# Kernel optimization log

Hardware: AMD Instinct MI355X
Metric: run time of the kernel (lower is better)

## Reference

```python
import jax, jax.numpy as jnp
import numpy as np

HIDDEN = 1024
HEADS = 16
HEAD_DIM = HIDDEN // HEADS


def setup_inputs() -> dict:
    key = jax.random.key(0)
    ks = jax.random.split(key, 12)
    B, S, D = 4, 2048, HIDDEN
    scale = 1.0 / np.sqrt(D)
    inp = {
        'q': jax.random.normal(ks[0], (B, S, D), jnp.float32),
        'k': jax.random.normal(ks[1], (B, S, D), jnp.float32),
        'v': jax.random.normal(ks[2], (B, S, D), jnp.float32),
        'Wq': jax.random.normal(ks[3], (D, D), jnp.float32) * scale,
        'bq': jnp.zeros((D,), jnp.float32),
        'Wk': jax.random.normal(ks[4], (D, D), jnp.float32) * scale,
        'bk': jnp.zeros((D,), jnp.float32),
        'Wv': jax.random.normal(ks[5], (D, D), jnp.float32) * scale,
        'bv': jnp.zeros((D,), jnp.float32),
        'Wo': jax.random.normal(ks[6], (D, D), jnp.float32) * scale,
        'bo': jnp.zeros((D,), jnp.float32),
    }
    return inp


def reference(q, k, v, Wq, bq, Wk, bk, Wv, bv, Wo, bo):
    B, S, D = q.shape
    H, Dh = HEADS, HEAD_DIM
    # QKV projections (weights stored as [in, out])
    Q = q @ Wq + bq
    K = k @ Wk + bk
    V = v @ Wv + bv
    # [B, H, S, Dh]
    Qh = Q.reshape(B, S, H, Dh).transpose(0, 2, 1, 3)
    Kh = K.reshape(B, S, H, Dh).transpose(0, 2, 1, 3)
    Vh = V.reshape(B, S, H, Dh).transpose(0, 2, 1, 3)
    # scaled dot-product attention, full [B,H,S,S] scores as in source
    scores = jnp.einsum('bhqd,bhkd->bhqk', Qh, Kh) / jnp.sqrt(jnp.float32(Dh))
    attn = jax.nn.softmax(scores, axis=-1)
    ctx = jnp.einsum('bhqk,bhkd->bhqd', attn, Vh)
    out = ctx.transpose(0, 2, 1, 3).reshape(B, S, D)
    return out @ Wo + bo
```

## Files before the change

### kernel.cpp

```cpp
#include <hip/hip_runtime.h>
#include <hip/hip_bf16.h>

#define HID 1024
#define NH 16
#define DH 64
#define NB 4
#define SQ 2048

typedef __bf16 bf16x8 __attribute__((ext_vector_type(8)));
typedef __bf16 bf16x2 __attribute__((ext_vector_type(2)));
typedef float f32x4 __attribute__((ext_vector_type(4)));
typedef float f32x16 __attribute__((ext_vector_type(16)));
typedef unsigned int u32x4 __attribute__((ext_vector_type(4)));

static __device__ __forceinline__ unsigned pkbf(float a, float b) {
  bf16x2 t; t[0] = (__bf16)a; t[1] = (__bf16)b;
  return __builtin_bit_cast(unsigned, t);
}

static __device__ __forceinline__ void gload16(const void* g, void* l) {
  __builtin_amdgcn_global_load_lds(
      (const __attribute__((address_space(1))) unsigned int*)g,
      (__attribute__((address_space(3))) unsigned int*)l, 16, 0, 0);
}

static __device__ __forceinline__ int xcd_swz(int lin, int nwg) {
  return (lin & 7) * (nwg >> 3) + (lin >> 3);
}

__global__ __launch_bounds__(256) void transpose_wf4_kernel(
    const float* __restrict__ Wq, const float* __restrict__ Wk,
    const float* __restrict__ Wv, const float* __restrict__ Wo,
    __bf16* __restrict__ Wcatf, __bf16* __restrict__ Wof) {
  const int which = blockIdx.z;
  const float* W = which == 0 ? Wq : (which == 1 ? Wk : (which == 2 ? Wv : Wo));
  __bf16* Wf = which == 3 ? Wof : Wcatf + (size_t)which * HID * HID;
  const int nblk = blockIdx.x, kt = blockIdx.y;
  const int tid = threadIdx.x, lane = tid & 63, wid = tid >> 6;
  const int fr = lane & 15, g = lane >> 4;
#pragma unroll
  for (int c = 0; c < 2; ++c) {
    const int wn_i = wid + c * 4;
    const int wn = wn_i >> 2, i = wn_i & 3;
    const int n = nblk * 128 + wn * 64 + i * 16 + fr;
    const int kb = kt * 32 + g * 8;
    bf16x8 v;
#pragma unroll
    for (int e = 0; e < 8; ++e)
      v[e] = (__bf16)W[(size_t)(kb + e) * HID + n];
    *reinterpret_cast<bf16x8*>(
        &Wf[(size_t)(nblk * 32 + kt) * 4096 + wn * 2048 + i * 512 + lane * 8]) = v;
  }
}

__global__ __launch_bounds__(256) void gemm_qkv_kernel(
    const float* __restrict__ Aq, const float* __restrict__ Ak,
    const float* __restrict__ Av, const __bf16* __restrict__ Wcatf,
    const float* __restrict__ bq, const float* __restrict__ bk,
    const float* __restrict__ bv, __bf16* __restrict__ Qh,
    __bf16* __restrict__ Kh, __bf16* __restrict__ Vt, float qscale) {
  const int K = HID;
  __shared__ __align__(16) char As2[2][10240];
  const int tid = threadIdx.x;
  const int lane = tid & 63;
  const int wid = tid >> 6;
  const int wm = wid >> 1, wn = wid & 1;
  const int lin = blockIdx.x + 24 * blockIdx.y;
  const int work = xcd_swz(lin, 1536);
  const int seg = work >> 9;
  const int rem = work & 511;
  const int m0 = (rem >> 3) * 128;
  const int nblk = seg * 8 + (rem & 7);
  const int n0 = nblk * 128;
  const int fr = lane & 15, g = lane >> 4;

  const float* Abase = seg == 0 ? Aq : (seg == 1 ? Ak : Av);
  const float* asrc =
      Abase + (size_t)(m0 + wid * 32 + (lane >> 3)) * K + (lane & 7) * 4;
  const __bf16* wsrc = Wcatf + (size_t)nblk * 32 * 4096 + wn * 2048 + lane * 8;

  const int awrow = wid * 32 + (lane >> 3);
  const int awcol = (lane & 7) * 8;

  float4 areg[4];
  auto loadA = [&](int kt) {
#pragma unroll
    for (int j = 0; j < 4; ++j)
      areg[j] = *reinterpret_cast<const float4*>(
          asrc + (size_t)j * 8 * K + kt * 32);
  };
  auto writeA = [&](int buf) {
#pragma unroll
    for (int j = 0; j < 4; ++j) {
      uint2 w;
      w.x = pkbf(areg[j].x, areg[j].y);
      w.y = pkbf(areg[j].z, areg[j].w);
      *reinterpret_cast<uint2*>(&As2[buf][(awrow + j * 8) * 80 + awcol]) = w;
    }
  };
  auto loadB = [&](int kt, bf16x8* br) {
    const __bf16* bp = wsrc + (size_t)kt * 4096;
#pragma unroll
    for (int i = 0; i < 4; ++i)
      br[i] = *reinterpret_cast<const bf16x8*>(bp + i * 512);
  };
  auto readA = [&](int buf, bf16x8* af) {
    const char* ac = &As2[buf][0];
#pragma unroll
    for (int i = 0; i < 4; ++i)
      af[i] = *reinterpret_cast<const bf16x8*>(
          ac + (wm * 64 + i * 16 + fr) * 80 + g * 16);
  };

  f32x4 acc[4][4] = {};
  const int NT = K / 32;
  bf16x8 bE[4], bO[4];
  loadA(0);
  writeA(0);
  loadB(0, bE);
  __syncthreads();
  int cur = 0;
  for (int kt = 0; kt < NT; kt += 2) {
    loadA(kt + 1);
    loadB(kt + 1, bO);
    {
      bf16x8 af[4];
      readA(cur, af);
#pragma unroll
      for (int i = 0; i < 4; ++i)
#pragma unroll
        for (int j = 0; j < 4; ++j)
          acc[i][j] = __builtin_amdgcn_mfma_f32_16x16x32_bf16(
              af[i], bE[j], acc[i][j], 0, 0, 0);
    }
    writeA(cur ^ 1);
    __syncthreads();
    cur ^= 1;
    if (kt + 2 < NT) {
      loadA(kt + 2);
      loadB(kt + 2, bE);
    }
    {
      bf16x8 af[4];
      readA(cur, af);
#pragma unroll
      for (int i = 0; i < 4; ++i)
#pragma unroll
        for (int j = 0; j < 4; ++j)
          acc[i][j] = __builtin_amdgcn_mfma_f32_16x16x32_bf16(
              af[i], bO[j], acc[i][j], 0, 0, 0);
    }
    if (kt + 2 < NT) {
      writeA(cur ^ 1);
      __syncthreads();
      cur ^= 1;
    }
  }

  const float* bias = seg == 0 ? bq : (seg == 1 ? bk : bv);
  const float oscale = seg == 0 ? qscale : 1.f;
#pragma unroll
  for (int i = 0; i < 4; ++i) {
#pragma unroll
    for (int j = 0; j < 4; ++j) {
      const int n = n0 + wn * 64 + j * 16 + fr;
      const int nn = n & 1023;
      const float bn = bias[nn];
      const int h = nn >> 6, dh = nn & (DH - 1);
#pragma unroll
      for (int r = 0; r < 4; ++r) {
        const int m = m0 + wm * 64 + i * 16 + g * 4 + r;
        const float v = (acc[i][j][r] + bn) * oscale;
        const int b = m >> 11, s = m & (SQ - 1);
        if (seg == 0) {
          Qh[(((size_t)(b * NH + h) * SQ) + s) * DH + dh] = (__bf16)v;
        } else if (seg == 1) {
          const int kvt = s >> 5, ql = s & 31;
          const int ds = dh >> 4, hi = (dh >> 3) & 1, e = dh & 7;
          Kh[(size_t)(b * NH + h) * SQ * DH +
             (size_t)kvt * 2048 + ds * 512 + (hi * 32 + ql) * 8 + e] = (__bf16)v;
        } else {
          const int i64 = s >> 6, c16 = (s >> 4) & 3;
          const int hi = (s >> 2) & 1, e = (s & 3) + 4 * ((s >> 3) & 1);
          const int dblk = dh >> 5, ql = dh & 31;
          Vt[(size_t)(b * NH + h) * SQ * DH +
             (size_t)i64 * 4096 + dblk * 2048 + c16 * 512 +
             (hi * 32 + ql) * 8 + e] = (__bf16)v;
        }
      }
    }
  }
}

__global__ __launch_bounds__(256) void gemm_out_kernel(
    const __bf16* __restrict__ Ap, const __bf16* __restrict__ Wof,
    const float* __restrict__ bias, float* __restrict__ out,
    int M, int N, int K) {
  __shared__ __align__(16) char Asm[2][8192];
  const int tid = threadIdx.x;
  const int lane = tid & 63;
  const int wid = tid >> 6;
  const int wm = wid >> 1, wn = wid & 1;
  const int gx = N / 128;
  const int lin = blockIdx.x + gx * blockIdx.y;
  const int work = xcd_swz(lin, gx * (M / 128));
  const int m0 = (work / gx) * 128, nblk = work % gx, n0 = nblk * 128;
  const int fr = lane & 15, g = lane >> 4, kg = (lane >> 4) * 8;

  const __bf16* abf = Ap + (size_t)(m0 + wid * 32 + (lane >> 2)) * K + (lane & 3) * 8;
  const __bf16* wsrc = Wof + (size_t)nblk * 32 * 4096 + wn * 2048 + lane * 8;

  auto stageA = [&](int buf, int kt) {
    char* ab = &Asm[buf][0] + wid * 2048;
#pragma unroll
    for (int j = 0; j < 2; ++j)
      gload16(abf + (size_t)j * 16 * K + kt * 32, ab + j * 1024);
  };
  auto loadB = [&](int kt, bf16x8* br) {
    const __bf16* bp = wsrc + (size_t)kt * 4096;
#pragma unroll
    for (int i = 0; i < 4; ++i)
      br[i] = *reinterpret_cast<const bf16x8*>(bp + i * 512);
  };
  auto readA = [&](int buf, bf16x8* af) {
    const char* ac = &Asm[buf][0];
#pragma unroll
    for (int i = 0; i < 4; ++i)
      af[i] = *reinterpret_cast<const bf16x8*>(
          ac + (wm * 64 + i * 16 + fr) * 64 + kg * 2);
  };

  f32x4 acc[4][4] = {};
  const int NT = K / 32;
  bf16x8 bE[4], bO[4];
  stageA(0, 0);
  loadB(0, bE);
  __syncthreads();
  int cur = 0;
  for (int kt = 0; kt < NT; kt += 2) {
    stageA(cur ^ 1, kt + 1);
    loadB(kt + 1, bO);
    {
      bf16x8 af[4];
      readA(cur, af);
#pragma unroll
      for (int i = 0; i < 4; ++i)
#pragma unroll
        for (int j = 0; j < 4; ++j)
          acc[i][j] = __builtin_amdgcn_mfma_f32_16x16x32_bf16(
              af[i], bE[j], acc[i][j], 0, 0, 0);
    }
    __syncthreads();
    cur ^= 1;
    if (kt + 2 < NT) {
      stageA(cur ^ 1, kt + 2);
      loadB(kt + 2, bE);
    }
    {
      bf16x8 af[4];
      readA(cur, af);
#pragma unroll
      for (int i = 0; i < 4; ++i)
#pragma unroll
        for (int j = 0; j < 4; ++j)
          acc[i][j] = __builtin_amdgcn_mfma_f32_16x16x32_bf16(
              af[i], bO[j], acc[i][j], 0, 0, 0);
    }
    if (kt + 2 < NT) {
      __syncthreads();
      cur ^= 1;
    }
  }

#pragma unroll
  for (int i = 0; i < 4; ++i) {
#pragma unroll
    for (int j = 0; j < 4; ++j) {
      const int n = n0 + wn * 64 + j * 16 + fr;
      const float bn = bias[n];
#pragma unroll
      for (int r = 0; r < 4; ++r) {
        const int m = m0 + wm * 64 + i * 16 + g * 4 + r;
        out[(size_t)m * N + n] = acc[i][j][r] + bn;
      }
    }
  }
}

__global__ __launch_bounds__(256) void attn_kernel(
    const __bf16* __restrict__ Q, const __bf16* __restrict__ K,
    const __bf16* __restrict__ V, __bf16* __restrict__ ctx) {
  __shared__ float tb[4][32][33];
  const int tid = threadIdx.x, lane = tid & 63, wid = tid >> 6;
  const int lin = blockIdx.x + 16 * blockIdx.y;
  const int work = xcd_swz(lin, 16 * NB * NH);
  const int bh = work >> 4;
  const int q0 = (work & 15) * 128 + wid * 32;
  const int ql = lane & 31, hi = lane >> 5;
  const __bf16* Qb = Q + (size_t)bh * SQ * DH;
  const __bf16* Kf = K + (size_t)bh * SQ * DH;
  const __bf16* Vf = V + (size_t)bh * SQ * DH;

  bf16x8 qf[4];
#pragma unroll
  for (int ds = 0; ds < 4; ++ds)
    qf[ds] = *reinterpret_cast<const bf16x8*>(
        &Qb[(size_t)(q0 + ql) * DH + ds * 16 + hi * 8]);

  f32x16 ot0 = {}, ot1 = {};
  float l_run = 0.f;

  for (int kv0 = 0; kv0 < SQ; kv0 += 64) {
    const __bf16* Ka = Kf + (size_t)(kv0 >> 5) * 2048 + lane * 8;
    const __bf16* Kc = Ka + 2048;
    bf16x8 kfa0 = *reinterpret_cast<const bf16x8*>(Ka);
    bf16x8 kfa1 = *reinterpret_cast<const bf16x8*>(Ka + 512);
    bf16x8 kfa2 = *reinterpret_cast<const bf16x8*>(Ka + 1024);
    bf16x8 kfa3 = *reinterpret_cast<const bf16x8*>(Ka + 1536);
    bf16x8 kfb0 = *reinterpret_cast<const bf16x8*>(Kc);
    bf16x8 kfb1 = *reinterpret_cast<const bf16x8*>(Kc + 512);
    bf16x8 kfb2 = *reinterpret_cast<const bf16x8*>(Kc + 1024);
    bf16x8 kfb3 = *reinterpret_cast<const bf16x8*>(Kc + 1536);
    const __bf16* Vbase = Vf + (size_t)(kv0 >> 6) * 4096 + lane * 8;
    bf16x8 v00a = *reinterpret_cast<const bf16x8*>(Vbase);
    bf16x8 v01a = *reinterpret_cast<const bf16x8*>(Vbase + 512);
    bf16x8 v00b = *reinterpret_cast<const bf16x8*>(Vbase + 1024);
    bf16x8 v01b = *reinterpret_cast<const bf16x8*>(Vbase + 1536);
    bf16x8 v10a = *reinterpret_cast<const bf16x8*>(Vbase + 2048);
    bf16x8 v11a = *reinterpret_cast<const bf16x8*>(Vbase + 2560);
    bf16x8 v10b = *reinterpret_cast<const bf16x8*>(Vbase + 3072);
    bf16x8 v11b = *reinterpret_cast<const bf16x8*>(Vbase + 3584);

    f32x16 sa = {}, sb = {};
    __builtin_amdgcn_s_setprio(1);
    sa = __builtin_amdgcn_mfma_f32_32x32x16_bf16(kfa0, qf[0], sa, 0, 0, 0);
    sb = __builtin_amdgcn_mfma_f32_32x32x16_bf16(kfb0, qf[0], sb, 0, 0, 0);
    sa = __builtin_amdgcn_mfma_f32_32x32x16_bf16(kfa1, qf[1], sa, 0, 0, 0);
    sb = __builtin_amdgcn_mfma_f32_32x32x16_bf16(kfb1, qf[1], sb, 0, 0, 0);
    sa = __builtin_amdgcn_mfma_f32_32x32x16_bf16(kfa2, qf[2], sa, 0, 0, 0);
    sb = __builtin_amdgcn_mfma_f32_32x32x16_bf16(kfb2, qf[2], sb, 0, 0, 0);
    sa = __builtin_amdgcn_mfma_f32_32x32x16_bf16(kfa3, qf[3], sa, 0, 0, 0);
    sb = __builtin_amdgcn_mfma_f32_32x32x16_bf16(kfb3, qf[3], sb, 0, 0, 0);
    __builtin_amdgcn_s_setprio(0);

    float pa[16], pb_[16];
#pragma unroll
    for (int r = 0; r < 16; ++r) pa[r] = __builtin_amdgcn_exp2f(sa[r]);
#pragma unroll
    for (int r = 0; r < 16; ++r) pb_[r] = __builtin_amdgcn_exp2f(sb[r]);
    {
      float u0 = 0.f, u1 = 0.f, u2 = 0.f, u3 = 0.f;
#pragma unroll
      for (int r = 0; r < 4; ++r) {
        u0 += pa[r] + pa[r + 4];
        u1 += pa[r + 8] + pa[r + 12];
        u2 += pb_[r] + pb_[r + 4];
        u3 += pb_[r + 8] + pb_[r + 12];
      }
      l_run += (u0 + u1) + (u2 + u3);
    }
    unsigned ca[8], cb[8];
#pragma unroll
    for (int i = 0; i < 8; ++i) {
      ca[i] = pkbf(pa[2 * i], pa[2 * i + 1]);
      cb[i] = pkbf(pb_[2 * i], pb_[2 * i + 1]);
    }
    u32x4 WA0, WA1, WB0, WB1;
    WA0[0] = ca[0]; WA0[1] = ca[1]; WA0[2] = ca[2]; WA0[3] = ca[3];
    WA1[0] = ca[4]; WA1[1] = ca[5]; WA1[2] = ca[6]; WA1[3] = ca[7];
    WB0[0] = cb[0]; WB0[1] = cb[1]; WB0[2] = cb[2]; WB0[3] = cb[3];
    WB1[0] = cb[4]; WB1[1] = cb[5]; WB1[2] = cb[6]; WB1[3] = cb[7];
    bf16x8 pa0 = __builtin_bit_cast(bf16x8, WA0);
    bf16x8 pa1 = __builtin_bit_cast(bf16x8, WA1);
    bf16x8 pb0 = __builtin_bit_cast(bf16x8, WB0);
    bf16x8 pb1 = __builtin_bit_cast(bf16x8, WB1);
    __builtin_amdgcn_s_setprio(1);
    ot0 = __builtin_amdgcn_mfma_f32_32x32x16_bf16(v00a, pa0, ot0, 0, 0, 0);
    ot1 = __builtin_amdgcn_mfma_f32_32x32x16_bf16(v10a, pa0, ot1, 0, 0, 0);
    ot0 = __builtin_amdgcn_mfma_f32_32x32x16_bf16(v01a, pa1, ot0, 0, 0, 0);
    ot1 = __builtin_amdgcn_mfma_f32_32x32x16_bf16(v11a, pa1, ot1, 0, 0, 0);
    ot0 = __builtin_amdgcn_mfma_f32_32x32x16_bf16(v00b, pb0, ot0, 0, 0, 0);
    ot1 = __builtin_amdgcn_mfma_f32_32x32x16_bf16(v10b, pb0, ot1, 0, 0, 0);
    ot0 = __builtin_amdgcn_mfma_f32_32x32x16_bf16(v01b, pb1, ot0, 0, 0, 0);
    ot1 = __builtin_amdgcn_mfma_f32_32x32x16_bf16(v11b, pb1, ot1, 0, 0, 0);
    __builtin_amdgcn_s_setprio(0);
  }
  l_run += __shfl_xor(l_run, 32);
  const float inv = 1.f / l_run;

  const int qr = lane >> 1, hf = lane & 1;
  const int b = bh >> 4, h = bh & 15;
  __bf16* dstb = ctx + ((size_t)(b * SQ + q0 + qr)) * HID + h * 64 + hf * 16;
#pragma unroll
  for (int r = 0; r < 16; ++r)
    tb[wid][ql][(r & 3) + 8 * (r >> 2) + 4 * hi] = ot0[r] * inv;
  {
    unsigned wb[8];
#pragma unroll
    for (int i = 0; i < 8; ++i)
      wb[i] = pkbf(tb[wid][qr][hf * 16 + 2 * i], tb[wid][qr][hf * 16 + 2 * i + 1]);
    u32x4 W0, W1;
    W0[0] = wb[0]; W0[1] = wb[1]; W0[2] = wb[2]; W0[3] = wb[3];
    W1[0] = wb[4]; W1[1] = wb[5]; W1[2] = wb[6]; W1[3] = wb[7];
    *reinterpret_cast<u32x4*>(dstb) = W0;
    *reinterpret_cast<u32x4*>(dstb + 8) = W1;
  }
  __builtin_amdgcn_s_waitcnt(0);
#pragma unroll
  for (int r = 0; r < 16; ++r)
    tb[wid][ql][(r & 3) + 8 * (r >> 2) + 4 * hi] = ot1[r] * inv;
  {
    unsigned wb[8];
#pragma unroll
    for (int i = 0; i < 8; ++i)
      wb[i] = pkbf(tb[wid][qr][hf * 16 + 2 * i], tb[wid][qr][hf * 16 + 2 * i + 1]);
    u32x4 W0, W1;
    W0[0] = wb[0]; W0[1] = wb[1]; W0[2] = wb[2]; W0[3] = wb[3];
    W1[0] = wb[4]; W1[1] = wb[5]; W1[2] = wb[6]; W1[3] = wb[7];
    *reinterpret_cast<u32x4*>(dstb + 32) = W0;
    *reinterpret_cast<u32x4*>(dstb + 40) = W1;
  }
}

extern "C" void kernel_launch(void* const* d_in, const int* in_sizes, int n_in,
                              void* d_out, int out_size, void* d_ws, size_t ws_size,
                              hipStream_t stream) {
  const float* q  = (const float*)d_in[0];
  const float* k  = (const float*)d_in[1];
  const float* v  = (const float*)d_in[2];
  const float* Wq = (const float*)d_in[3];
  const float* bq = (const float*)d_in[4];
  const float* Wk = (const float*)d_in[5];
  const float* bk = (const float*)d_in[6];
  const float* Wv = (const float*)d_in[7];
  const float* bv = (const float*)d_in[8];
  const float* Wo = (const float*)d_in[9];
  const float* bo = (const float*)d_in[10];

  char* ws = (char*)d_ws;
  const size_t WSZ = (size_t)HID * HID * 2;
  const size_t QSZ = (size_t)NB * NH * SQ * DH * 2;
  __bf16* Wcatf = (__bf16*)(ws);
  __bf16* Wof  = (__bf16*)(ws + 3 * WSZ);
  __bf16* Qh   = (__bf16*)(ws + 4 * WSZ);
  __bf16* Kh   = (__bf16*)(ws + 4 * WSZ + QSZ);
  __bf16* Vt   = (__bf16*)(ws + 4 * WSZ + 2 * QSZ);
  __bf16* ctxb = (__bf16*)(ws + 4 * WSZ + 3 * QSZ);

  const int M = NB * SQ;
  const float qscale = 0.125f * 1.44269504088896f;

  transpose_wf4_kernel<<<dim3(8, 32, 4), 256, 0, stream>>>(
      Wq, Wk, Wv, Wo, Wcatf, Wof);

  gemm_qkv_kernel<<<dim3(24, 64), 256, 0, stream>>>(
      q, k, v, Wcatf, bq, bk, bv, Qh, Kh, Vt, qscale);

  attn_kernel<<<dim3(SQ / 128, NB * NH), 256, 0, stream>>>(Qh, Kh, Vt, ctxb);

  gemm_out_kernel<<<dim3(HID / 128, M / 128), 256, 0, stream>>>(
      ctxb, Wof, bo, (float*)d_out, M, HID, HID);
}
```

Baseline: 218.8 us.

## Pre-convert QKV activations to bf16 and stage GEMM A tiles via direct LDS loads

Adds a separate kernel that converts the q, k and v activations from fp32 to bf16 into workspace. The QKV GEMM then reads bf16 A tiles with global_load_lds straight into an unpadded LDS buffer, instead of loading fp32 into registers, converting and writing to LDS. This is meant to halve A-tile bytes inside the GEMM and remove conversion and register staging from its main loop. In exchange it adds a full extra pass over all three activation tensors plus a workspace write, and the unpadded 64-byte LDS row stride may cause bank conflicts in the fragment reads.

```diff
diff --git a/kernel.cpp b/kernel.cpp
--- a/kernel.cpp
+++ b/kernel.cpp
@@ -53,14 +53,33 @@
   }
 }
 
+__global__ __launch_bounds__(256) void cvt_a_kernel(
+    const float* __restrict__ q, const float* __restrict__ k,
+    const float* __restrict__ v, __bf16* __restrict__ Abf) {
+  const int which = blockIdx.y;
+  const float* src = which == 0 ? q : (which == 1 ? k : v);
+  __bf16* dst = Abf + (size_t)which * ((size_t)NB * SQ * HID);
+  const size_t base = ((size_t)blockIdx.x * 256 + threadIdx.x) * 16;
+  float4 f0 = *reinterpret_cast<const float4*>(src + base);
+  float4 f1 = *reinterpret_cast<const float4*>(src + base + 4);
+  float4 f2 = *reinterpret_cast<const float4*>(src + base + 8);
+  float4 f3 = *reinterpret_cast<const float4*>(src + base + 12);
+  u32x4 w0, w1;
+  w0[0] = pkbf(f0.x, f0.y); w0[1] = pkbf(f0.z, f0.w);
+  w0[2] = pkbf(f1.x, f1.y); w0[3] = pkbf(f1.z, f1.w);
+  w1[0] = pkbf(f2.x, f2.y); w1[1] = pkbf(f2.z, f2.w);
+  w1[2] = pkbf(f3.x, f3.y); w1[3] = pkbf(f3.z, f3.w);
+  *reinterpret_cast<u32x4*>(dst + base) = w0;
+  *reinterpret_cast<u32x4*>(dst + base + 8) = w1;
+}
+
 __global__ __launch_bounds__(256) void gemm_qkv_kernel(
-    const float* __restrict__ Aq, const float* __restrict__ Ak,
-    const float* __restrict__ Av, const __bf16* __restrict__ Wcatf,
+    const __bf16* __restrict__ Abf, const __bf16* __restrict__ Wcatf,
     const float* __restrict__ bq, const float* __restrict__ bk,
     const float* __restrict__ bv, __bf16* __restrict__ Qh,
     __bf16* __restrict__ Kh, __bf16* __restrict__ Vt, float qscale) {
   const int K = HID;
-  __shared__ __align__(16) char As2[2][10240];
+  __shared__ __align__(16) char Asm[2][8192];
   const int tid = threadIdx.x;
   const int lane = tid & 63;
   const int wid = tid >> 6;
@@ -72,31 +91,18 @@
   const int m0 = (rem >> 3) * 128;
   const int nblk = seg * 8 + (rem & 7);
   const int n0 = nblk * 128;
-  const int fr = lane & 15, g = lane >> 4;
-
-  const float* Abase = seg == 0 ? Aq : (seg == 1 ? Ak : Av);
-  const float* asrc =
-      Abase + (size_t)(m0 + wid * 32 + (lane >> 3)) * K + (lane & 7) * 4;
+  const int fr = lane & 15, g = lane >> 4, kg = (lane >> 4) * 8;
+
+  const __bf16* Ap = Abf + (size_t)seg * ((size_t)NB * SQ) * K;
+  const __bf16* abf =
+      Ap + (size_t)(m0 + wid * 32 + (lane >> 2)) * K + (lane & 3) * 8;
   const __bf16* wsrc = Wcatf + (size_t)nblk * 32 * 4096 + wn * 2048 + lane * 8;
 
-  const int awrow = wid * 32 + (lane >> 3);
-  const int awcol = (lane & 7) * 8;
-
-  float4 areg[4];
-  auto loadA = [&](int kt) {
-#pragma unroll
-    for (int j = 0; j < 4; ++j)
-      areg[j] = *reinterpret_cast<const float4*>(
-          asrc + (size_t)j * 8 * K + kt * 32);
-  };
-  auto writeA = [&](int buf) {
-#pragma unroll
-    for (int j = 0; j < 4; ++j) {
-      uint2 w;
-      w.x = pkbf(areg[j].x, areg[j].y);
-      w.y = pkbf(areg[j].z, areg[j].w);
-      *reinterpret_cast<uint2*>(&As2[buf][(awrow + j * 8) * 80 + awcol]) = w;
-    }
+  auto stageA = [&](int buf, int kt) {
+    char* ab = &Asm[buf][0] + wid * 2048;
+#pragma unroll
+    for (int j = 0; j < 2; ++j)
+      gload16(abf + (size_t)j * 16 * K + kt * 32, ab + j * 1024);
   };
   auto loadB = [&](int kt, bf16x8* br) {
     const __bf16* bp = wsrc + (size_t)kt * 4096;
@@ -105,23 +111,22 @@
       br[i] = *reinterpret_cast<const bf16x8*>(bp + i * 512);
   };
   auto readA = [&](int buf, bf16x8* af) {
-    const char* ac = &As2[buf][0];
+    const char* ac = &Asm[buf][0];
 #pragma unroll
     for (int i = 0; i < 4; ++i)
       af[i] = *reinterpret_cast<const bf16x8*>(
-          ac + (wm * 64 + i * 16 + fr) * 80 + g * 16);
+          ac + (wm * 64 + i * 16 + fr) * 64 + kg * 2);
   };
 
   f32x4 acc[4][4] = {};
   const int NT = K / 32;
   bf16x8 bE[4], bO[4];
-  loadA(0);
-  writeA(0);
+  stageA(0, 0);
   loadB(0, bE);
   __syncthreads();
   int cur = 0;
   for (int kt = 0; kt < NT; kt += 2) {
-    loadA(kt + 1);
+    stageA(cur ^ 1, kt + 1);
     loadB(kt + 1, bO);
     {
       bf16x8 af[4];
@@ -133,11 +138,10 @@
           acc[i][j] = __builtin_amdgcn_mfma_f32_16x16x32_bf16(
               af[i], bE[j], acc[i][j], 0, 0, 0);
     }
-    writeA(cur ^ 1);
     __syncthreads();
     cur ^= 1;
     if (kt + 2 < NT) {
-      loadA(kt + 2);
+      stageA(cur ^ 1, kt + 2);
       loadB(kt + 2, bE);
     }
     {
@@ -151,7 +155,6 @@
               af[i], bO[j], acc[i][j], 0, 0, 0);
     }
     if (kt + 2 < NT) {
-      writeA(cur ^ 1);
       __syncthreads();
       cur ^= 1;
     }
@@ -446,15 +449,19 @@
   __bf16* Kh   = (__bf16*)(ws + 4 * WSZ + QSZ);
   __bf16* Vt   = (__bf16*)(ws + 4 * WSZ + 2 * QSZ);
   __bf16* ctxb = (__bf16*)(ws + 4 * WSZ + 3 * QSZ);
+  __bf16* Abf  = (__bf16*)(ws + 4 * WSZ + 4 * QSZ);
 
   const int M = NB * SQ;
   const float qscale = 0.125f * 1.44269504088896f;
 
+  cvt_a_kernel<<<dim3((size_t)NB * SQ * HID / 4096, 3), 256, 0, stream>>>(
+      q, k, v, Abf);
+
   transpose_wf4_kernel<<<dim3(8, 32, 4), 256, 0, stream>>>(
       Wq, Wk, Wv, Wo, Wcatf, Wof);
 
   gemm_qkv_kernel<<<dim3(24, 64), 256, 0, stream>>>(
-      q, k, v, Wcatf, bq, bk, bv, Qh, Kh, Vt, qscale);
+      Abf, Wcatf, bq, bk, bv, Qh, Kh, Vt, qscale);
 
   attn_kernel<<<dim3(SQ / 128, NB * NH), 256, 0, stream>>>(Qh, Kh, Vt, ctxb);
 
```

Result: slower. 236.5 us (+8.1%).
